# Kernel optimization log

Hardware: AMD Instinct MI355X
Metric: run time of the kernel (lower is better)

Reference implementation:

```python
import jax, jax.numpy as jnp
import numpy as np

DIM = 384
HEADS = 6
HEAD_DIM = DIM // HEADS
MLP_DIM = int(DIM * 4.0)
EPS = 1e-5


def layer_norm(x, g, b):
    mu = jnp.mean(x, axis=-1, keepdims=True)
    var = jnp.mean(jnp.square(x - mu), axis=-1, keepdims=True)
    return (x - mu) * jax.lax.rsqrt(var + EPS) * g + b


def setup_inputs() -> dict:
    key = jax.random.key(0)
    ks = jax.random.split(key, 12)
    s = 0.02
    return {
        "x": jax.random.normal(ks[0], (8, 2048, DIM), dtype=jnp.float32),
        "ln1_g": jnp.ones((DIM,), jnp.float32),
        "ln1_b": jnp.zeros((DIM,), jnp.float32),
        "qkv_w": jax.random.normal(ks[1], (DIM, 3 * DIM), jnp.float32) * s,
        "qkv_b": jnp.zeros((3 * DIM,), jnp.float32),
        "proj_w": jax.random.normal(ks[2], (DIM, DIM), jnp.float32) * s,
        "proj_b": jnp.zeros((DIM,), jnp.float32),
        "ln2_g": jnp.ones((DIM,), jnp.float32),
        "ln2_b": jnp.zeros((DIM,), jnp.float32),
        "fc1_w": jax.random.normal(ks[3], (DIM, MLP_DIM), jnp.float32) * s,
        "fc1_b": jnp.zeros((MLP_DIM,), jnp.float32),
        "fc2_w": jax.random.normal(ks[4], (MLP_DIM, DIM), jnp.float32) * s,
        "fc2_b": jnp.zeros((DIM,), jnp.float32),
    }


def reference(x, ln1_g, ln1_b, qkv_w, qkv_b, proj_w, proj_b,
              ln2_g, ln2_b, fc1_w, fc1_b, fc2_w, fc2_b):
    B, N, C = x.shape
    # --- attention ---
    h = layer_norm(x, ln1_g, ln1_b)
    qkv = h @ qkv_w + qkv_b  # [B,N,3C]
    qkv = qkv.reshape(B, N, 3, HEADS, HEAD_DIM)
    q, k, v = jnp.moveaxis(qkv, 2, 0)  # each [B,N,H,D]
    scale = HEAD_DIM ** -0.5
    attn = jnp.einsum('bnhd,bmhd->bhnm', q, k) * scale  # [B,H,N,N]
    attn = jax.nn.softmax(attn, axis=-1)
    o = jnp.einsum('bhnm,bmhd->bnhd', attn, v).reshape(B, N, C)
    x = x + o @ proj_w + proj_b
    # --- mlp ---
    h = layer_norm(x, ln2_g, ln2_b)
    h = jax.nn.gelu(h @ fc1_w + fc1_b, approximate=False)
    x = x + h @ fc2_w + fc2_b
    return x
```

## Files before the change

kernel.cpp:

```cpp
#include <hip/hip_runtime.h>
#include <hip/hip_bf16.h>

#define DIM   384
#define SEQ   2048
#define BATCH 8
#define NHEAD 6
#define HD    64
#define MLPD  1536
#define MTOT  (BATCH*SEQ)

typedef __attribute__((ext_vector_type(8))) short bf16x8;
typedef __attribute__((ext_vector_type(4))) float f32x4;

static __device__ __forceinline__ float bf2f(unsigned short u){
    union { float f; unsigned int i; } v; v.i = ((unsigned int)u) << 16; return v.f;
}
static __device__ __forceinline__ unsigned short f2bf(float f){
    union { float f; unsigned int i; } v; v.f = f;
    unsigned int r = v.i + 0x7fffu + ((v.i >> 16) & 1u);
    return (unsigned short)(r >> 16);
}
static __device__ __forceinline__ unsigned int asu(float f){
    union { float f; unsigned int i; } v; v.f = f; return v.i;
}
static __device__ __forceinline__ void gload_lds16(const unsigned short* g, unsigned short* l){
    __builtin_amdgcn_global_load_lds(
        (__attribute__((address_space(1))) void*)(g),
        (__attribute__((address_space(3))) void*)(l), 16, 0, 0);
}

__global__ __launch_bounds__(256) void wt_all_kernel(
    const float* __restrict__ qkv_w, const float* __restrict__ proj_w,
    const float* __restrict__ fc1_w, const float* __restrict__ fc2_w,
    unsigned short* __restrict__ o_qkv, unsigned short* __restrict__ o_prj,
    unsigned short* __restrict__ o_fc1, unsigned short* __restrict__ o_fc2)
{
    __shared__ float tile[64][68];
    int bid = blockIdx.x;
    const float* W; unsigned short* Wt; int K, N, tk, tn;
    if (bid < 108)      { W = qkv_w; Wt = o_qkv; K = 384;  N = 1152; tk = bid/18;        tn = bid%18; }
    else if (bid < 144) { W = proj_w; Wt = o_prj; K = 384;  N = 384;  tk = (bid-108)/6;  tn = (bid-108)%6; }
    else if (bid < 288) { W = fc1_w; Wt = o_fc1; K = 384;  N = 1536; tk = (bid-144)/24; tn = (bid-144)%24; }
    else                { W = fc2_w; Wt = o_fc2; K = 1536; N = 384;  tk = (bid-288)/6;  tn = (bid-288)%6; }
    int t = threadIdx.x;
    int lr = t >> 4, lc = (t & 15) * 4;
#pragma unroll
    for (int p = 0; p < 4; p++){
        float4 v = *(const float4*)(W + (size_t)(tk*64 + p*16 + lr) * N + tn*64 + lc);
        *(float4*)&tile[p*16 + lr][lc] = v;
    }
    __syncthreads();
    int n = t >> 2, k0 = (t & 3) * 16;
    unsigned int w[8];
#pragma unroll
    for (int i = 0; i < 8; i++)
        w[i] = (unsigned int)f2bf(tile[k0 + 2*i][n]) | ((unsigned int)f2bf(tile[k0 + 2*i + 1][n]) << 16);
    unsigned short* dst = Wt + (size_t)(tn*64 + n) * K + tk*64 + k0;
    *(uint4*)(dst)     = make_uint4(w[0], w[1], w[2], w[3]);
    *(uint4*)(dst + 8) = make_uint4(w[4], w[5], w[6], w[7]);
}

__global__ __launch_bounds__(256) void ln_kernel(const float* __restrict__ x,
                                                 const float* __restrict__ g,
                                                 const float* __restrict__ b,
                                                 unsigned short* __restrict__ out){
    int row  = blockIdx.x * 4 + (threadIdx.x >> 6);
    int lane = threadIdx.x & 63;
    const float* xr = x + (size_t)row * DIM;
    float v[6];
#pragma unroll
    for (int p = 0; p < 3; p++){
        float2 t = *(const float2*)(xr + lane * 2 + p * 128);
        v[2*p] = t.x; v[2*p+1] = t.y;
    }
    float s = 0.f, sq = 0.f;
#pragma unroll
    for (int i = 0; i < 6; i++){ s += v[i]; sq += v[i] * v[i]; }
#pragma unroll
    for (int off = 1; off < 64; off <<= 1){
        s  += __shfl_xor(s, off);
        sq += __shfl_xor(sq, off);
    }
    float mu   = s * (1.0f / DIM);
    float var  = sq * (1.0f / DIM) - mu * mu;
    float rstd = rsqrtf(var + 1e-5f);
    unsigned short* orow = out + (size_t)row * DIM;
#pragma unroll
    for (int p = 0; p < 3; p++){
        int c = lane * 2 + p * 128;
        float h0 = (v[2*p]   - mu) * rstd * g[c]   + b[c];
        float h1 = (v[2*p+1] - mu) * rstd * g[c+1] + b[c+1];
        unsigned int pk = (unsigned int)f2bf(h0) | ((unsigned int)f2bf(h1) << 16);
        *(unsigned int*)(orow + c) = pk;
    }
}

template<int EPI>
__global__ __launch_bounds__(128, 3) void gemm_kernel(
    const unsigned short* __restrict__ A, const unsigned short* __restrict__ Bt,
    const float* __restrict__ bias, int K, int N,
    const float* __restrict__ resid, float* __restrict__ outf,
    unsigned short* __restrict__ outb,
    unsigned short* __restrict__ qb, unsigned short* __restrict__ kb2,
    unsigned short* __restrict__ vb)
{
    __shared__ __align__(16) unsigned short smem[64*64 + 128*64];
    unsigned short* As = smem;
    unsigned short* Bs = smem + 64*64;
    int t = threadIdx.x;
    int wid = t >> 6, lane = t & 63, quad = lane >> 4, l15 = lane & 15;
    int row0 = blockIdx.y * 64, col0 = blockIdx.x * 128;
    int sr = lane >> 3, sc = lane & 7;
    int scl = (sc ^ sr) * 8;

    const unsigned short* Ab = A  + (size_t)row0 * K;
    const unsigned short* Bb = Bt + (size_t)col0 * K;

    f32x4 acc[2][8];
    f32x4 zz = {0.f, 0.f, 0.f, 0.f};
#pragma unroll
    for (int i = 0; i < 2; i++)
#pragma unroll
        for (int j = 0; j < 8; j++) acc[i][j] = zz;

    for (int k0 = 0; k0 < K; k0 += 64){
        __syncthreads();
#pragma unroll
        for (int jj = 0; jj < 4; jj++){
            int rb = wid * 32 + jj * 8;
            gload_lds16(Ab + (size_t)(rb + sr) * K + k0 + scl, &As[rb * 64]);
        }
#pragma unroll
        for (int jj = 0; jj < 8; jj++){
            int rb = wid * 64 + jj * 8;
            gload_lds16(Bb + (size_t)(rb + sr) * K + k0 + scl, &Bs[rb * 64]);
        }
        __syncthreads();
#pragma unroll
        for (int kk = 0; kk < 2; kk++){
            bf16x8 af[2], bf[8];
#pragma unroll
            for (int i = 0; i < 2; i++){
                int r = wid*32 + i*16 + l15;
                af[i] = *(const bf16x8*)&As[r * 64 + (((kk*4 + quad) ^ (l15 & 7)) * 8)];
            }
#pragma unroll
            for (int j = 0; j < 8; j++){
                int r = j*16 + l15;
                bf[j] = *(const bf16x8*)&Bs[r * 64 + (((kk*4 + quad) ^ (l15 & 7)) * 8)];
            }
#pragma unroll
            for (int i = 0; i < 2; i++)
#pragma unroll
                for (int j = 0; j < 8; j++)
                    acc[i][j] = __builtin_amdgcn_mfma_f32_16x16x32_bf16(af[i], bf[j], acc[i][j], 0, 0, 0);
        }
    }

    if (EPI == 0 && col0 >= 768){
        __syncthreads();
        unsigned short* T = smem;
#pragma unroll
        for (int i = 0; i < 2; i++)
#pragma unroll
            for (int j = 0; j < 8; j++){
                int gcl = j*16 + l15;
                float bia = bias[col0 + gcl];
                int nsl0 = wid*32 + i*16 + quad*4;
#pragma unroll
                for (int r = 0; r < 4; r++)
                    T[gcl * 72 + nsl0 + r] = f2bf(acc[i][j][r] + bia);
            }
        __syncthreads();
        int rem = (col0 - 768) + t;
        int head = rem >> 6, d = rem & 63;
        int bidx = row0 >> 11, ns0 = row0 & 2047;
        unsigned short* dst = vb + ((size_t)((bidx * NHEAD + head) * 64 + d)) * SEQ + ns0;
        const unsigned short* src = T + t * 72;
#pragma unroll
        for (int m = 0; m < 8; m++)
            *(uint4*)(dst + m*8) = *(const uint4*)(src + m*8);
        return;
    }

#pragma unroll
    for (int i = 0; i < 2; i++){
#pragma unroll
        for (int j = 0; j < 8; j++){
            int gr0 = row0 + wid*32 + i*16 + quad*4;
            int gc  = col0 + j*16 + l15;
            float bia = bias[gc];
#pragma unroll
            for (int r = 0; r < 4; r++){
                int gr = gr0 + r;
                float val = acc[i][j][r] + bia;
                if (EPI == 1){
                    outf[(size_t)gr * N + gc] = resid[(size_t)gr * N + gc] + val;
                } else if (EPI == 2){
                    float u = val * (1.0f + 0.044715f * val * val);
                    float e = __builtin_amdgcn_exp2f(u * 2.3025851f);
                    outb[(size_t)gr * N + gc] = f2bf(val * e / (e + 1.0f));
                } else {
                    int trip = gc / 384, remq = gc - trip * 384;
                    int head = remq >> 6, d = remq & 63;
                    int bidx = gr >> 11, ns = gr & 2047;
                    size_t off = ((size_t)(bidx * NHEAD + head) * SEQ + ns) * 64 + d;
                    unsigned short* dstp = (trip == 0) ? qb : kb2;
                    dstp[off] = f2bf(val);
                }
            }
        }
    }
}

__global__ __launch_bounds__(128, 3) void attn_kernel(const unsigned short* __restrict__ Q,
                                                      const unsigned short* __restrict__ Kb,
                                                      const unsigned short* __restrict__ Vt,
                                                      unsigned short* __restrict__ O){
    __shared__ __align__(16) unsigned short Ks[64 * 64];
    __shared__ __align__(16) unsigned short Vs[64 * 64];
    __shared__ __align__(16) unsigned short Ps[2][32 * 64];

    int bh = blockIdx.y, qt = blockIdx.x;
    int t = threadIdx.x, wid = t >> 6, lane = t & 63, quad = lane >> 4, l15 = lane & 15;
    int l7 = l15 & 7;
    int q0 = qt * 64 + wid * 32;
    const unsigned short* Qp = Q  + (size_t)bh * SEQ * 64;
    const unsigned short* Kp = Kb + (size_t)bh * SEQ * 64;
    const unsigned short* Vp = Vt + (size_t)bh * 64 * SEQ;
    int sr = lane >> 3, sc = lane & 7;
    int scl = (sc ^ sr) * 8;

    const float QSCALE = 0.125f * 1.44269504f;
    bf16x8 qf[2][2];
#pragma unroll
    for (int h = 0; h < 2; h++){
#pragma unroll
        for (int c = 0; c < 2; c++){
            union { uint4 u; unsigned short s[8]; } cv;
            cv.u = *(const uint4*)(Qp + (size_t)(q0 + h*16 + l15) * 64 + c * 32 + quad * 8);
            bf16x8 f;
#pragma unroll
            for (int j = 0; j < 8; j++) f[j] = (short)f2bf(bf2f(cv.s[j]) * QSCALE);
            qf[h][c] = f;
        }
    }

    bf16x8 ones;
#pragma unroll
    for (int j = 0; j < 8; j++) ones[j] = (short)0x3F80;

    f32x4 oacc[2][4], sacc[2];
    f32x4 zz = {0.f, 0.f, 0.f, 0.f};
#pragma unroll
    for (int h = 0; h < 2; h++){
        sacc[h] = zz;
#pragma unroll
        for (int dn = 0; dn < 4; dn++) oacc[h][dn] = zz;
    }
    unsigned short* P = &Ps[wid][0];

    const unsigned short* kf_ptr[4][2];
#pragma unroll
    for (int n = 0; n < 4; n++){
        int kv = n * 16 + l15;
        kf_ptr[n][0] = &Ks[kv * 64 + ((quad       ^ (kv & 7)) * 8)];
        kf_ptr[n][1] = &Ks[kv * 64 + (((4 + quad) ^ (kv & 7)) * 8)];
    }
    const unsigned short* vf_ptr[2][4];
#pragma unroll
    for (int c = 0; c < 2; c++)
#pragma unroll
        for (int dn = 0; dn < 4; dn++){
            int d = dn * 16 + l15;
            vf_ptr[c][dn] = &Vs[d * 64 + (((c*4 + quad) ^ (d & 7)) * 8)];
        }
    const unsigned short* pf_ptr[2][2];
#pragma unroll
    for (int c = 0; c < 2; c++)
#pragma unroll
        for (int h = 0; h < 2; h++)
            pf_ptr[c][h] = P + (h*16 + l15) * 64 + (((c*4 + quad) ^ l7) * 8);
    uint2* pw_ptr[2][4];
#pragma unroll
    for (int h = 0; h < 2; h++)
#pragma unroll
        for (int n = 0; n < 4; n++){
            int qloc = h * 16 + l15;
            int chunk = n * 2 + (quad >> 1);
            pw_ptr[h][n] = (uint2*)(P + qloc * 64 + ((chunk ^ l7) * 8) + (quad & 1) * 4);
        }
    const unsigned short* kstage[4];
    const unsigned short* vstage[4];
    unsigned short* klds[4];
    unsigned short* vlds[4];
#pragma unroll
    for (int jj = 0; jj < 4; jj++){
        int rb = wid * 32 + jj * 8;
        kstage[jj] = Kp + (size_t)(rb + sr) * 64 + scl;
        vstage[jj] = Vp + (size_t)(rb + sr) * SEQ + scl;
        klds[jj] = &Ks[rb * 64];
        vlds[jj] = &Vs[rb * 64];
    }

    for (int kt = 0; kt < SEQ / 64; kt++){
        __syncthreads();
#pragma unroll
        for (int jj = 0; jj < 4; jj++){
            gload_lds16(kstage[jj], klds[jj]);
            gload_lds16(vstage[jj], vlds[jj]);
            kstage[jj] += 64 * 64;
            vstage[jj] += 64;
        }
        __syncthreads();

        f32x4 st[2][4];
#pragma unroll
        for (int n = 0; n < 4; n++){
            bf16x8 kf0 = *(const bf16x8*)kf_ptr[n][0];
            bf16x8 kf1 = *(const bf16x8*)kf_ptr[n][1];
#pragma unroll
            for (int h = 0; h < 2; h++){
                f32x4 z = __builtin_amdgcn_mfma_f32_16x16x32_bf16(kf0, qf[h][0], zz, 0, 0, 0);
                st[h][n] = __builtin_amdgcn_mfma_f32_16x16x32_bf16(kf1, qf[h][1], z, 0, 0, 0);
            }
        }

#pragma unroll
        for (int h = 0; h < 2; h++){
#pragma unroll
            for (int n = 0; n < 4; n++){
                float p0 = __builtin_amdgcn_exp2f(st[h][n][0]);
                float p1 = __builtin_amdgcn_exp2f(st[h][n][1]);
                float p2 = __builtin_amdgcn_exp2f(st[h][n][2]);
                float p3 = __builtin_amdgcn_exp2f(st[h][n][3]);
                unsigned int w0 = __builtin_amdgcn_perm(asu(p1), asu(p0), 0x07060302u);
                unsigned int w1 = __builtin_amdgcn_perm(asu(p3), asu(p2), 0x07060302u);
                *pw_ptr[h][n] = make_uint2(w0, w1);
            }
        }

        asm volatile("s_waitcnt lgkmcnt(0)" ::: "memory");

#pragma unroll
        for (int c = 0; c < 2; c++){
            bf16x8 pf[2];
#pragma unroll
            for (int h = 0; h < 2; h++)
                pf[h] = *(const bf16x8*)pf_ptr[c][h];
            sacc[0] = __builtin_amdgcn_mfma_f32_16x16x32_bf16(ones, pf[0], sacc[0], 0, 0, 0);
            sacc[1] = __builtin_amdgcn_mfma_f32_16x16x32_bf16(ones, pf[1], sacc[1], 0, 0, 0);
#pragma unroll
            for (int dn = 0; dn < 4; dn++){
                bf16x8 vf = *(const bf16x8*)vf_ptr[c][dn];
                oacc[0][dn] = __builtin_amdgcn_mfma_f32_16x16x32_bf16(vf, pf[0], oacc[0][dn], 0, 0, 0);
                oacc[1][dn] = __builtin_amdgcn_mfma_f32_16x16x32_bf16(vf, pf[1], oacc[1][dn], 0, 0, 0);
            }
        }
    }

    int b = bh / NHEAD, hh = bh - b * NHEAD;
#pragma unroll
    for (int h = 0; h < 2; h++){
        float rd = 1.0f / sacc[h][0];
        size_t row = (size_t)(b * SEQ + q0 + h*16 + l15);
#pragma unroll
        for (int dn = 0; dn < 4; dn++){
            float v0 = oacc[h][dn][0] * rd, v1 = oacc[h][dn][1] * rd;
            float v2 = oacc[h][dn][2] * rd, v3 = oacc[h][dn][3] * rd;
            unsigned int w0 = (unsigned int)f2bf(v0) | ((unsigned int)f2bf(v1) << 16);
            unsigned int w1 = (unsigned int)f2bf(v2) | ((unsigned int)f2bf(v3) << 16);
            *(uint2*)(O + row * DIM + hh * 64 + dn * 16 + quad * 4) = make_uint2(w0, w1);
        }
    }
}

extern "C" void kernel_launch(void* const* d_in, const int* in_sizes, int n_in,
                              void* d_out, int out_size, void* d_ws, size_t ws_size,
                              hipStream_t stream){
    const float* x      = (const float*)d_in[0];
    const float* ln1_g  = (const float*)d_in[1];
    const float* ln1_b  = (const float*)d_in[2];
    const float* qkv_w  = (const float*)d_in[3];
    const float* qkv_b  = (const float*)d_in[4];
    const float* proj_w = (const float*)d_in[5];
    const float* proj_b = (const float*)d_in[6];
    const float* ln2_g  = (const float*)d_in[7];
    const float* ln2_b  = (const float*)d_in[8];
    const float* fc1_w  = (const float*)d_in[9];
    const float* fc1_b  = (const float*)d_in[10];
    const float* fc2_w  = (const float*)d_in[11];
    const float* fc2_b  = (const float*)d_in[12];
    float* out = (float*)d_out;

    char* p = (char*)d_ws;
    auto take = [&](size_t n){ char* r = p; p += (n + 255) & ~(size_t)255; return r; };
    unsigned short* wt_qkv = (unsigned short*)take((size_t)1152 * 384 * 2);
    unsigned short* wt_prj = (unsigned short*)take((size_t)384 * 384 * 2);
    unsigned short* wt_fc1 = (unsigned short*)take((size_t)1536 * 384 * 2);
    unsigned short* wt_fc2 = (unsigned short*)take((size_t)384 * 1536 * 2);
    unsigned short* rbig   = (unsigned short*)take((size_t)MTOT * 4 * DIM * 2);
    unsigned short* h2     = (unsigned short*)take((size_t)MTOT * DIM * 2);
    float*          x1     = (float*)take((size_t)MTOT * DIM * 4);

    unsigned short* h1     = rbig;
    unsigned short* qb     = rbig + (size_t)MTOT * DIM;
    unsigned short* kb     = qb   + (size_t)MTOT * DIM;
    unsigned short* vb     = kb   + (size_t)MTOT * DIM;
    unsigned short* attn_o = rbig;
    unsigned short* hm     = rbig;

    wt_all_kernel<<<dim3(432), 256, 0, stream>>>(qkv_w, proj_w, fc1_w, fc2_w,
                                                 wt_qkv, wt_prj, wt_fc1, wt_fc2);
    ln_kernel<<<dim3(MTOT/4), 256, 0, stream>>>(x, ln1_g, ln1_b, h1);
    gemm_kernel<0><<<dim3(9, 256), 128, 0, stream>>>(h1, wt_qkv, qkv_b, 384, 1152,
                                                     nullptr, nullptr, nullptr, qb, kb, vb);
    attn_kernel<<<dim3(SEQ/64, BATCH*NHEAD), 128, 0, stream>>>(qb, kb, vb, attn_o);
    gemm_kernel<1><<<dim3(3, 256), 128, 0, stream>>>(attn_o, wt_prj, proj_b, 384, 384,
                                                     x, x1, nullptr, nullptr, nullptr, nullptr);
    ln_kernel<<<dim3(MTOT/4), 256, 0, stream>>>(x1, ln2_g, ln2_b, h2);
    gemm_kernel<2><<<dim3(12, 256), 128, 0, stream>>>(h2, wt_fc1, fc1_b, 384, 1536,
                                                      nullptr, nullptr, hm, nullptr, nullptr, nullptr);
    gemm_kernel<1><<<dim3(3, 256), 128, 0, stream>>>(hm, wt_fc2, fc2_b, 1536, 384,
                                                     x1, out, nullptr, nullptr, nullptr, nullptr);
}
```

Measured before the change: 299.0 us.

## Double-buffer LDS staging in GEMM and attention kernels with async prefetch

Both the GEMM and attention main loops now use two LDS buffers. The next K/V or A/B tile is issued with global_load_lds before computing on the current one, and explicit vmcnt waits plus raw barriers replace the two __syncthreads per iteration. K becomes a template parameter so the loop can be fully structured into pairs of stages. This aims to hide global-memory latency behind MFMA work. In exchange it doubles LDS use per block (48KB for the GEMM), which may limit occupancy.

```diff
diff --git a/kernel.cpp b/kernel.cpp
--- a/kernel.cpp
+++ b/kernel.cpp
@@ -28,6 +28,12 @@
         (__attribute__((address_space(1))) void*)(g),
         (__attribute__((address_space(3))) void*)(l), 16, 0, 0);
 }
+static __device__ __forceinline__ void barx(){
+    asm volatile("" ::: "memory");
+    __builtin_amdgcn_s_barrier();
+    asm volatile("" ::: "memory");
+}
+#define WAITVM(N) asm volatile("s_waitcnt vmcnt(" #N ")" ::: "memory")
 
 __global__ __launch_bounds__(256) void wt_all_kernel(
     const float* __restrict__ qkv_w, const float* __restrict__ proj_w,
@@ -95,26 +101,60 @@
     }
 }
 
-template<int EPI>
+template<int OFF>
+static __device__ __forceinline__ void gemm_tile(const unsigned short* smem,
+                                                 int wid, int quad, int l15,
+                                                 f32x4 acc[2][8])
+{
+#pragma unroll
+    for (int kk = 0; kk < 2; kk++){
+        bf16x8 af[2], bf[8];
+#pragma unroll
+        for (int i = 0; i < 2; i++){
+            int r = wid*32 + i*16 + l15;
+            af[i] = *(const bf16x8*)&smem[OFF + r * 64 + (((kk*4 + quad) ^ (l15 & 7)) * 8)];
+        }
+#pragma unroll
+        for (int j = 0; j < 8; j++){
+            int r = j*16 + l15;
+            bf[j] = *(const bf16x8*)&smem[OFF + 4096 + r * 64 + (((kk*4 + quad) ^ (l15 & 7)) * 8)];
+        }
+#pragma unroll
+        for (int i = 0; i < 2; i++)
+#pragma unroll
+            for (int j = 0; j < 8; j++)
+                acc[i][j] = __builtin_amdgcn_mfma_f32_16x16x32_bf16(af[i], bf[j], acc[i][j], 0, 0, 0);
+    }
+}
+
+template<int EPI, int K>
 __global__ __launch_bounds__(128, 3) void gemm_kernel(
     const unsigned short* __restrict__ A, const unsigned short* __restrict__ Bt,
-    const float* __restrict__ bias, int K, int N,
+    const float* __restrict__ bias, int N,
     const float* __restrict__ resid, float* __restrict__ outf,
     unsigned short* __restrict__ outb,
     unsigned short* __restrict__ qb, unsigned short* __restrict__ kb2,
     unsigned short* __restrict__ vb)
 {
-    __shared__ __align__(16) unsigned short smem[64*64 + 128*64];
-    unsigned short* As = smem;
-    unsigned short* Bs = smem + 64*64;
+    __shared__ __align__(16) unsigned short smem[2 * 12288];
     int t = threadIdx.x;
     int wid = t >> 6, lane = t & 63, quad = lane >> 4, l15 = lane & 15;
     int row0 = blockIdx.y * 64, col0 = blockIdx.x * 128;
     int sr = lane >> 3, sc = lane & 7;
     int scl = (sc ^ sr) * 8;
 
-    const unsigned short* Ab = A  + (size_t)row0 * K;
-    const unsigned short* Bb = Bt + (size_t)col0 * K;
+    const unsigned short* A0 = A  + (size_t)(row0 + wid*32 + sr) * K + scl;
+    const unsigned short* B0 = Bt + (size_t)(col0 + wid*64 + sr) * K + scl;
+    int kc = 0;
+
+#define GSTAGE(LOFF) do { \
+    _Pragma("unroll") \
+    for (int jj = 0; jj < 4; jj++) \
+        gload_lds16(A0 + jj*8*K + kc, &smem[(LOFF) + (wid*32 + jj*8) * 64]); \
+    _Pragma("unroll") \
+    for (int jj = 0; jj < 8; jj++) \
+        gload_lds16(B0 + jj*8*K + kc, &smem[(LOFF) + 4096 + (wid*64 + jj*8) * 64]); \
+    kc += 64; } while(0)
 
     f32x4 acc[2][8];
     f32x4 zz = {0.f, 0.f, 0.f, 0.f};
@@ -123,39 +163,29 @@
 #pragma unroll
         for (int j = 0; j < 8; j++) acc[i][j] = zz;
 
-    for (int k0 = 0; k0 < K; k0 += 64){
-        __syncthreads();
-#pragma unroll
-        for (int jj = 0; jj < 4; jj++){
-            int rb = wid * 32 + jj * 8;
-            gload_lds16(Ab + (size_t)(rb + sr) * K + k0 + scl, &As[rb * 64]);
-        }
-#pragma unroll
-        for (int jj = 0; jj < 8; jj++){
-            int rb = wid * 64 + jj * 8;
-            gload_lds16(Bb + (size_t)(rb + sr) * K + k0 + scl, &Bs[rb * 64]);
-        }
-        __syncthreads();
-#pragma unroll
-        for (int kk = 0; kk < 2; kk++){
-            bf16x8 af[2], bf[8];
-#pragma unroll
-            for (int i = 0; i < 2; i++){
-                int r = wid*32 + i*16 + l15;
-                af[i] = *(const bf16x8*)&As[r * 64 + (((kk*4 + quad) ^ (l15 & 7)) * 8)];
-            }
-#pragma unroll
-            for (int j = 0; j < 8; j++){
-                int r = j*16 + l15;
-                bf[j] = *(const bf16x8*)&Bs[r * 64 + (((kk*4 + quad) ^ (l15 & 7)) * 8)];
-            }
-#pragma unroll
-            for (int i = 0; i < 2; i++)
-#pragma unroll
-                for (int j = 0; j < 8; j++)
-                    acc[i][j] = __builtin_amdgcn_mfma_f32_16x16x32_bf16(af[i], bf[j], acc[i][j], 0, 0, 0);
-        }
-    }
+    GSTAGE(0);
+    constexpr int PAIRS = K / 128;
+    for (int p = 0; p < PAIRS - 1; p++){
+        GSTAGE(12288);
+        WAITVM(12);
+        barx();
+        gemm_tile<0>(smem, wid, quad, l15, acc);
+        barx();
+        GSTAGE(0);
+        WAITVM(12);
+        barx();
+        gemm_tile<12288>(smem, wid, quad, l15, acc);
+        barx();
+    }
+    GSTAGE(12288);
+    WAITVM(12);
+    barx();
+    gemm_tile<0>(smem, wid, quad, l15, acc);
+    barx();
+    WAITVM(0);
+    barx();
+    gemm_tile<12288>(smem, wid, quad, l15, acc);
+#undef GSTAGE
 
     if (EPI == 0 && col0 >= 768){
         __syncthreads();
@@ -213,13 +243,63 @@
     }
 }
 
+template<int LOFF>
+static __device__ __forceinline__ void attn_tile(
+    const bf16x8 (&qf)[2][2], const bf16x8& ones,
+    const unsigned short* const (&kf_ptr)[4][2],
+    const unsigned short* const (&vf_ptr)[2][4],
+    const unsigned short* const (&pf_ptr)[2][2],
+    uint2* const (&pw_ptr)[2][4],
+    f32x4 (&sacc)[2], f32x4 (&oacc)[2][4])
+{
+    const f32x4 zz = {0.f, 0.f, 0.f, 0.f};
+    f32x4 st[2][4];
+#pragma unroll
+    for (int n = 0; n < 4; n++){
+        bf16x8 kf0 = *(const bf16x8*)(kf_ptr[n][0] + LOFF);
+        bf16x8 kf1 = *(const bf16x8*)(kf_ptr[n][1] + LOFF);
+#pragma unroll
+        for (int h = 0; h < 2; h++){
+            f32x4 z = __builtin_amdgcn_mfma_f32_16x16x32_bf16(kf0, qf[h][0], zz, 0, 0, 0);
+            st[h][n] = __builtin_amdgcn_mfma_f32_16x16x32_bf16(kf1, qf[h][1], z, 0, 0, 0);
+        }
+    }
+#pragma unroll
+    for (int h = 0; h < 2; h++){
+#pragma unroll
+        for (int n = 0; n < 4; n++){
+            float p0 = __builtin_amdgcn_exp2f(st[h][n][0]);
+            float p1 = __builtin_amdgcn_exp2f(st[h][n][1]);
+            float p2 = __builtin_amdgcn_exp2f(st[h][n][2]);
+            float p3 = __builtin_amdgcn_exp2f(st[h][n][3]);
+            unsigned int w0 = __builtin_amdgcn_perm(asu(p1), asu(p0), 0x07060302u);
+            unsigned int w1 = __builtin_amdgcn_perm(asu(p3), asu(p2), 0x07060302u);
+            *pw_ptr[h][n] = make_uint2(w0, w1);
+        }
+    }
+    asm volatile("s_waitcnt lgkmcnt(0)" ::: "memory");
+#pragma unroll
+    for (int c = 0; c < 2; c++){
+        bf16x8 pf[2];
+#pragma unroll
+        for (int h = 0; h < 2; h++)
+            pf[h] = *(const bf16x8*)pf_ptr[c][h];
+        sacc[0] = __builtin_amdgcn_mfma_f32_16x16x32_bf16(ones, pf[0], sacc[0], 0, 0, 0);
+        sacc[1] = __builtin_amdgcn_mfma_f32_16x16x32_bf16(ones, pf[1], sacc[1], 0, 0, 0);
+#pragma unroll
+        for (int dn = 0; dn < 4; dn++){
+            bf16x8 vf = *(const bf16x8*)(vf_ptr[c][dn] + LOFF);
+            oacc[0][dn] = __builtin_amdgcn_mfma_f32_16x16x32_bf16(vf, pf[0], oacc[0][dn], 0, 0, 0);
+            oacc[1][dn] = __builtin_amdgcn_mfma_f32_16x16x32_bf16(vf, pf[1], oacc[1][dn], 0, 0, 0);
+        }
+    }
+}
+
 __global__ __launch_bounds__(128, 3) void attn_kernel(const unsigned short* __restrict__ Q,
                                                       const unsigned short* __restrict__ Kb,
                                                       const unsigned short* __restrict__ Vt,
                                                       unsigned short* __restrict__ O){
-    __shared__ __align__(16) unsigned short Ks[64 * 64];
-    __shared__ __align__(16) unsigned short Vs[64 * 64];
-    __shared__ __align__(16) unsigned short Ps[2][32 * 64];
+    __shared__ __align__(16) unsigned short smem[2*4096 + 2*4096 + 2*2048];
 
     int bh = blockIdx.y, qt = blockIdx.x;
     int t = threadIdx.x, wid = t >> 6, lane = t & 63, quad = lane >> 4, l15 = lane & 15;
@@ -258,14 +338,14 @@
 #pragma unroll
         for (int dn = 0; dn < 4; dn++) oacc[h][dn] = zz;
     }
-    unsigned short* P = &Ps[wid][0];
+    unsigned short* P = &smem[16384 + wid * 2048];
 
     const unsigned short* kf_ptr[4][2];
 #pragma unroll
     for (int n = 0; n < 4; n++){
         int kv = n * 16 + l15;
-        kf_ptr[n][0] = &Ks[kv * 64 + ((quad       ^ (kv & 7)) * 8)];
-        kf_ptr[n][1] = &Ks[kv * 64 + (((4 + quad) ^ (kv & 7)) * 8)];
+        kf_ptr[n][0] = &smem[kv * 64 + ((quad       ^ (kv & 7)) * 8)];
+        kf_ptr[n][1] = &smem[kv * 64 + (((4 + quad) ^ (kv & 7)) * 8)];
     }
     const unsigned short* vf_ptr[2][4];
 #pragma unroll
@@ -273,7 +353,7 @@
 #pragma unroll
         for (int dn = 0; dn < 4; dn++){
             int d = dn * 16 + l15;
-            vf_ptr[c][dn] = &Vs[d * 64 + (((c*4 + quad) ^ (d & 7)) * 8)];
+            vf_ptr[c][dn] = &smem[8192 + d * 64 + (((c*4 + quad) ^ (d & 7)) * 8)];
         }
     const unsigned short* pf_ptr[2][2];
 #pragma unroll
@@ -299,65 +379,41 @@
         int rb = wid * 32 + jj * 8;
         kstage[jj] = Kp + (size_t)(rb + sr) * 64 + scl;
         vstage[jj] = Vp + (size_t)(rb + sr) * SEQ + scl;
-        klds[jj] = &Ks[rb * 64];
-        vlds[jj] = &Vs[rb * 64];
-    }
-
-    for (int kt = 0; kt < SEQ / 64; kt++){
-        __syncthreads();
-#pragma unroll
-        for (int jj = 0; jj < 4; jj++){
-            gload_lds16(kstage[jj], klds[jj]);
-            gload_lds16(vstage[jj], vlds[jj]);
-            kstage[jj] += 64 * 64;
-            vstage[jj] += 64;
-        }
-        __syncthreads();
-
-        f32x4 st[2][4];
-#pragma unroll
-        for (int n = 0; n < 4; n++){
-            bf16x8 kf0 = *(const bf16x8*)kf_ptr[n][0];
-            bf16x8 kf1 = *(const bf16x8*)kf_ptr[n][1];
-#pragma unroll
-            for (int h = 0; h < 2; h++){
-                f32x4 z = __builtin_amdgcn_mfma_f32_16x16x32_bf16(kf0, qf[h][0], zz, 0, 0, 0);
-                st[h][n] = __builtin_amdgcn_mfma_f32_16x16x32_bf16(kf1, qf[h][1], z, 0, 0, 0);
-            }
-        }
-
-#pragma unroll
-        for (int h = 0; h < 2; h++){
-#pragma unroll
-            for (int n = 0; n < 4; n++){
-                float p0 = __builtin_amdgcn_exp2f(st[h][n][0]);
-                float p1 = __builtin_amdgcn_exp2f(st[h][n][1]);
-                float p2 = __builtin_amdgcn_exp2f(st[h][n][2]);
-                float p3 = __builtin_amdgcn_exp2f(st[h][n][3]);
-                unsigned int w0 = __builtin_amdgcn_perm(asu(p1), asu(p0), 0x07060302u);
-                unsigned int w1 = __builtin_amdgcn_perm(asu(p3), asu(p2), 0x07060302u);
-                *pw_ptr[h][n] = make_uint2(w0, w1);
-            }
-        }
-
-        asm volatile("s_waitcnt lgkmcnt(0)" ::: "memory");
-
-#pragma unroll
-        for (int c = 0; c < 2; c++){
-            bf16x8 pf[2];
-#pragma unroll
-            for (int h = 0; h < 2; h++)
-                pf[h] = *(const bf16x8*)pf_ptr[c][h];
-            sacc[0] = __builtin_amdgcn_mfma_f32_16x16x32_bf16(ones, pf[0], sacc[0], 0, 0, 0);
-            sacc[1] = __builtin_amdgcn_mfma_f32_16x16x32_bf16(ones, pf[1], sacc[1], 0, 0, 0);
-#pragma unroll
-            for (int dn = 0; dn < 4; dn++){
-                bf16x8 vf = *(const bf16x8*)vf_ptr[c][dn];
-                oacc[0][dn] = __builtin_amdgcn_mfma_f32_16x16x32_bf16(vf, pf[0], oacc[0][dn], 0, 0, 0);
-                oacc[1][dn] = __builtin_amdgcn_mfma_f32_16x16x32_bf16(vf, pf[1], oacc[1][dn], 0, 0, 0);
-            }
-        }
-    }
+        klds[jj] = &smem[rb * 64];
+        vlds[jj] = &smem[8192 + rb * 64];
+    }
+
+#define AISSUE(BOFF) do { \
+    _Pragma("unroll") \
+    for (int jj = 0; jj < 4; jj++){ \
+        gload_lds16(kstage[jj], klds[jj] + (BOFF)); \
+        gload_lds16(vstage[jj], vlds[jj] + (BOFF)); \
+        kstage[jj] += 64 * 64; \
+        vstage[jj] += 64; \
+    } } while(0)
+
+    AISSUE(0);
+    for (int p = 0; p < SEQ/128 - 1; p++){
+        AISSUE(4096);
+        WAITVM(8);
+        barx();
+        attn_tile<0>(qf, ones, kf_ptr, vf_ptr, pf_ptr, pw_ptr, sacc, oacc);
+        barx();
+        AISSUE(0);
+        WAITVM(8);
+        barx();
+        attn_tile<4096>(qf, ones, kf_ptr, vf_ptr, pf_ptr, pw_ptr, sacc, oacc);
+        barx();
+    }
+    AISSUE(4096);
+    WAITVM(8);
+    barx();
+    attn_tile<0>(qf, ones, kf_ptr, vf_ptr, pf_ptr, pw_ptr, sacc, oacc);
+    barx();
+    WAITVM(0);
+    barx();
+    attn_tile<4096>(qf, ones, kf_ptr, vf_ptr, pf_ptr, pw_ptr, sacc, oacc);
+#undef AISSUE
 
     int b = bh / NHEAD, hh = bh - b * NHEAD;
 #pragma unroll
@@ -413,14 +469,14 @@
     wt_all_kernel<<<dim3(432), 256, 0, stream>>>(qkv_w, proj_w, fc1_w, fc2_w,
                                                  wt_qkv, wt_prj, wt_fc1, wt_fc2);
     ln_kernel<<<dim3(MTOT/4), 256, 0, stream>>>(x, ln1_g, ln1_b, h1);
-    gemm_kernel<0><<<dim3(9, 256), 128, 0, stream>>>(h1, wt_qkv, qkv_b, 384, 1152,
+    gemm_kernel<0,384><<<dim3(9, 256), 128, 0, stream>>>(h1, wt_qkv, qkv_b, 1152,
                                                      nullptr, nullptr, nullptr, qb, kb, vb);
     attn_kernel<<<dim3(SEQ/64, BATCH*NHEAD), 128, 0, stream>>>(qb, kb, vb, attn_o);
-    gemm_kernel<1><<<dim3(3, 256), 128, 0, stream>>>(attn_o, wt_prj, proj_b, 384, 384,
+    gemm_kernel<1,384><<<dim3(3, 256), 128, 0, stream>>>(attn_o, wt_prj, proj_b, 384,
                                                      x, x1, nullptr, nullptr, nullptr, nullptr);
     ln_kernel<<<dim3(MTOT/4), 256, 0, stream>>>(x1, ln2_g, ln2_b, h2);
-    gemm_kernel<2><<<dim3(12, 256), 128, 0, stream>>>(h2, wt_fc1, fc1_b, 384, 1536,
+    gemm_kernel<2,384><<<dim3(12, 256), 128, 0, stream>>>(h2, wt_fc1, fc1_b, 1536,
                                                       nullptr, nullptr, hm, nullptr, nullptr, nullptr);
-    gemm_kernel<1><<<dim3(3, 256), 128, 0, stream>>>(hm, wt_fc2, fc2_b, 1536, 384,
+    gemm_kernel<1,1536><<<dim3(3, 256), 128, 0, stream>>>(hm, wt_fc2, fc2_b, 384,
                                                      x1, out, nullptr, nullptr, nullptr, nullptr);
 }
```

Measured after the change: 322.8 us. 8.0% more time.

## Prefetch next K/V tile into registers to overlap loads with attention compute

Applied to the files above, without the earlier changes.

Replaces the direct global-to-LDS loads in the attention loop with a register-staged software pipeline. The next K/V tile is loaded into registers while the current tile is computed, then written to LDS after a barrier. This is meant to hide global memory latency behind the MFMA and exp work. It costs extra VGPRs for the staged tiles, which may lower occupancy under the launch bounds of 3 blocks, and it adds explicit vmcnt waits and barriers.

```diff
diff --git a/kernel.cpp b/kernel.cpp
--- a/kernel.cpp
+++ b/kernel.cpp
@@ -28,6 +28,12 @@
         (__attribute__((address_space(1))) void*)(g),
         (__attribute__((address_space(3))) void*)(l), 16, 0, 0);
 }
+static __device__ __forceinline__ void barx(){
+    asm volatile("" ::: "memory");
+    __builtin_amdgcn_s_barrier();
+    asm volatile("" ::: "memory");
+}
+#define WAITVM(N) asm volatile("s_waitcnt vmcnt(" #N ")" ::: "memory")
 
 __global__ __launch_bounds__(256) void wt_all_kernel(
     const float* __restrict__ qkv_w, const float* __restrict__ proj_w,
@@ -213,13 +219,62 @@
     }
 }
 
+static __device__ __forceinline__ void attn_tile(
+    const bf16x8 (&qf)[2][2], const bf16x8& ones,
+    const unsigned short* const (&kf_ptr)[4][2],
+    const unsigned short* const (&vf_ptr)[2][4],
+    const unsigned short* const (&pf_ptr)[2][2],
+    uint2* const (&pw_ptr)[2][4],
+    f32x4 (&sacc)[2], f32x4 (&oacc)[2][4])
+{
+    const f32x4 zz = {0.f, 0.f, 0.f, 0.f};
+    f32x4 st[2][4];
+#pragma unroll
+    for (int n = 0; n < 4; n++){
+        bf16x8 kf0 = *(const bf16x8*)kf_ptr[n][0];
+        bf16x8 kf1 = *(const bf16x8*)kf_ptr[n][1];
+#pragma unroll
+        for (int h = 0; h < 2; h++){
+            f32x4 z = __builtin_amdgcn_mfma_f32_16x16x32_bf16(kf0, qf[h][0], zz, 0, 0, 0);
+            st[h][n] = __builtin_amdgcn_mfma_f32_16x16x32_bf16(kf1, qf[h][1], z, 0, 0, 0);
+        }
+    }
+#pragma unroll
+    for (int h = 0; h < 2; h++){
+#pragma unroll
+        for (int n = 0; n < 4; n++){
+            float p0 = __builtin_amdgcn_exp2f(st[h][n][0]);
+            float p1 = __builtin_amdgcn_exp2f(st[h][n][1]);
+            float p2 = __builtin_amdgcn_exp2f(st[h][n][2]);
+            float p3 = __builtin_amdgcn_exp2f(st[h][n][3]);
+            unsigned int w0 = __builtin_amdgcn_perm(asu(p1), asu(p0), 0x07060302u);
+            unsigned int w1 = __builtin_amdgcn_perm(asu(p3), asu(p2), 0x07060302u);
+            *pw_ptr[h][n] = make_uint2(w0, w1);
+        }
+    }
+    asm volatile("s_waitcnt lgkmcnt(0)" ::: "memory");
+#pragma unroll
+    for (int c = 0; c < 2; c++){
+        bf16x8 pf[2];
+#pragma unroll
+        for (int h = 0; h < 2; h++)
+            pf[h] = *(const bf16x8*)pf_ptr[c][h];
+        sacc[0] = __builtin_amdgcn_mfma_f32_16x16x32_bf16(ones, pf[0], sacc[0], 0, 0, 0);
+        sacc[1] = __builtin_amdgcn_mfma_f32_16x16x32_bf16(ones, pf[1], sacc[1], 0, 0, 0);
+#pragma unroll
+        for (int dn = 0; dn < 4; dn++){
+            bf16x8 vf = *(const bf16x8*)vf_ptr[c][dn];
+            oacc[0][dn] = __builtin_amdgcn_mfma_f32_16x16x32_bf16(vf, pf[0], oacc[0][dn], 0, 0, 0);
+            oacc[1][dn] = __builtin_amdgcn_mfma_f32_16x16x32_bf16(vf, pf[1], oacc[1][dn], 0, 0, 0);
+        }
+    }
+}
+
 __global__ __launch_bounds__(128, 3) void attn_kernel(const unsigned short* __restrict__ Q,
                                                       const unsigned short* __restrict__ Kb,
                                                       const unsigned short* __restrict__ Vt,
                                                       unsigned short* __restrict__ O){
-    __shared__ __align__(16) unsigned short Ks[64 * 64];
-    __shared__ __align__(16) unsigned short Vs[64 * 64];
-    __shared__ __align__(16) unsigned short Ps[2][32 * 64];
+    __shared__ __align__(16) unsigned short smem[4096 + 4096 + 2*2048];
 
     int bh = blockIdx.y, qt = blockIdx.x;
     int t = threadIdx.x, wid = t >> 6, lane = t & 63, quad = lane >> 4, l15 = lane & 15;
@@ -258,14 +313,14 @@
 #pragma unroll
         for (int dn = 0; dn < 4; dn++) oacc[h][dn] = zz;
     }
-    unsigned short* P = &Ps[wid][0];
+    unsigned short* P = &smem[8192 + wid * 2048];
 
     const unsigned short* kf_ptr[4][2];
 #pragma unroll
     for (int n = 0; n < 4; n++){
         int kv = n * 16 + l15;
-        kf_ptr[n][0] = &Ks[kv * 64 + ((quad       ^ (kv & 7)) * 8)];
-        kf_ptr[n][1] = &Ks[kv * 64 + (((4 + quad) ^ (kv & 7)) * 8)];
+        kf_ptr[n][0] = &smem[kv * 64 + ((quad       ^ (kv & 7)) * 8)];
+        kf_ptr[n][1] = &smem[kv * 64 + (((4 + quad) ^ (kv & 7)) * 8)];
     }
     const unsigned short* vf_ptr[2][4];
 #pragma unroll
@@ -273,7 +328,7 @@
 #pragma unroll
         for (int dn = 0; dn < 4; dn++){
             int d = dn * 16 + l15;
-            vf_ptr[c][dn] = &Vs[d * 64 + (((c*4 + quad) ^ (d & 7)) * 8)];
+            vf_ptr[c][dn] = &smem[4096 + d * 64 + (((c*4 + quad) ^ (d & 7)) * 8)];
         }
     const unsigned short* pf_ptr[2][2];
 #pragma unroll
@@ -292,71 +347,48 @@
         }
     const unsigned short* kstage[4];
     const unsigned short* vstage[4];
-    unsigned short* klds[4];
-    unsigned short* vlds[4];
+    uint4* kw[4];
+    uint4* vw[4];
 #pragma unroll
     for (int jj = 0; jj < 4; jj++){
         int rb = wid * 32 + jj * 8;
         kstage[jj] = Kp + (size_t)(rb + sr) * 64 + scl;
         vstage[jj] = Vp + (size_t)(rb + sr) * SEQ + scl;
-        klds[jj] = &Ks[rb * 64];
-        vlds[jj] = &Vs[rb * 64];
+        kw[jj] = (uint4*)(&smem[rb * 64] + (size_t)lane * 8);
+        vw[jj] = (uint4*)(&smem[4096 + rb * 64] + (size_t)lane * 8);
+    }
+
+    uint4 kreg[4], vreg[4];
+#pragma unroll
+    for (int jj = 0; jj < 4; jj++){
+        kreg[jj] = *(const uint4*)kstage[jj];
+        vreg[jj] = *(const uint4*)vstage[jj];
+        kstage[jj] += 64 * 64;
+        vstage[jj] += 64;
     }
 
     for (int kt = 0; kt < SEQ / 64; kt++){
-        __syncthreads();
+        WAITVM(0);
+        barx();
 #pragma unroll
         for (int jj = 0; jj < 4; jj++){
-            gload_lds16(kstage[jj], klds[jj]);
-            gload_lds16(vstage[jj], vlds[jj]);
-            kstage[jj] += 64 * 64;
-            vstage[jj] += 64;
-        }
-        __syncthreads();
-
-        f32x4 st[2][4];
-#pragma unroll
-        for (int n = 0; n < 4; n++){
-            bf16x8 kf0 = *(const bf16x8*)kf_ptr[n][0];
-            bf16x8 kf1 = *(const bf16x8*)kf_ptr[n][1];
-#pragma unroll
-            for (int h = 0; h < 2; h++){
-                f32x4 z = __builtin_amdgcn_mfma_f32_16x16x32_bf16(kf0, qf[h][0], zz, 0, 0, 0);
-                st[h][n] = __builtin_amdgcn_mfma_f32_16x16x32_bf16(kf1, qf[h][1], z, 0, 0, 0);
+            *kw[jj] = kreg[jj];
+            *vw[jj] = vreg[jj];
+        }
+        if (kt < SEQ / 64 - 1){
+#pragma unroll
+            for (int jj = 0; jj < 4; jj++){
+                kreg[jj] = *(const uint4*)kstage[jj];
+                vreg[jj] = *(const uint4*)vstage[jj];
+                kstage[jj] += 64 * 64;
+                vstage[jj] += 64;
             }
         }
-
-#pragma unroll
-        for (int h = 0; h < 2; h++){
-#pragma unroll
-            for (int n = 0; n < 4; n++){
-                float p0 = __builtin_amdgcn_exp2f(st[h][n][0]);
-                float p1 = __builtin_amdgcn_exp2f(st[h][n][1]);
-                float p2 = __builtin_amdgcn_exp2f(st[h][n][2]);
-                float p3 = __builtin_amdgcn_exp2f(st[h][n][3]);
-                unsigned int w0 = __builtin_amdgcn_perm(asu(p1), asu(p0), 0x07060302u);
-                unsigned int w1 = __builtin_amdgcn_perm(asu(p3), asu(p2), 0x07060302u);
-                *pw_ptr[h][n] = make_uint2(w0, w1);
-            }
-        }
-
+        __builtin_amdgcn_sched_barrier(0);
         asm volatile("s_waitcnt lgkmcnt(0)" ::: "memory");
-
-#pragma unroll
-        for (int c = 0; c < 2; c++){
-            bf16x8 pf[2];
-#pragma unroll
-            for (int h = 0; h < 2; h++)
-                pf[h] = *(const bf16x8*)pf_ptr[c][h];
-            sacc[0] = __builtin_amdgcn_mfma_f32_16x16x32_bf16(ones, pf[0], sacc[0], 0, 0, 0);
-            sacc[1] = __builtin_amdgcn_mfma_f32_16x16x32_bf16(ones, pf[1], sacc[1], 0, 0, 0);
-#pragma unroll
-            for (int dn = 0; dn < 4; dn++){
-                bf16x8 vf = *(const bf16x8*)vf_ptr[c][dn];
-                oacc[0][dn] = __builtin_amdgcn_mfma_f32_16x16x32_bf16(vf, pf[0], oacc[0][dn], 0, 0, 0);
-                oacc[1][dn] = __builtin_amdgcn_mfma_f32_16x16x32_bf16(vf, pf[1], oacc[1][dn], 0, 0, 0);
-            }
-        }
+        __builtin_amdgcn_s_barrier();
+        asm volatile("" ::: "memory");
+        attn_tile(qf, ones, kf_ptr, vf_ptr, pf_ptr, pw_ptr, sacc, oacc);
     }
 
     int b = bh / NHEAD, hh = bh - b * NHEAD;
```

Measured after the change: 439.2 us. 1.47x slower.
